# Performance work log

Measured on AMD Instinct MI355X. Metric: run time of the kernel, lower is better.

## Reference

```python
import jax, jax.numpy as jnp
import numpy as np
from jax import lax

# Static config (matches init_kwargs / electrode montage)
B, T, V = 16, 1536, 64
F1, D, H = 16, 2, 4
F2 = F1 * D              # 32
FO = F2 // H             # 8, GAT per-head out dim
K1, K3 = 32, 16          # conv kernel sizes (temporal)
P1, P2 = 8, 4            # avg pool sizes
KNN = 4
EPS = 1e-5
NEG_SLOPE = 0.2          # PyG GATConv leaky_relu slope


def _build_edges():
    # deterministic electrode geometry -> kNN graph, plus PyG self-loops
    rng = np.random.RandomState(0)
    pos = rng.randn(V, 3)
    dmat = np.linalg.norm(pos[:, None] - pos[None, :], axis=-1)
    order = np.argsort(dmat, axis=1)
    nbrs = order[:, 1:KNN + 1]                      # exclude self
    src = np.repeat(np.arange(V), KNN)
    dst = nbrs.reshape(-1)
    # add self loops (GATConv default add_self_loops=True)
    src = np.concatenate([src, np.arange(V)])
    dst = np.concatenate([dst, np.arange(V)])
    return jnp.asarray(np.stack([src, dst]), dtype=jnp.int32)  # (2, E)


def _bn(x, g, b, m, v, axis):
    shp = [1] * x.ndim
    shp[axis] = -1
    rs = lambda a: a.reshape(shp)
    return rs(g) * (x - rs(m)) * lax.rsqrt(rs(v) + EPS) + rs(b)


def _conv_same_t(x, w, k):
    # Conv2d(..., (1,k), padding='same'): torch pads (k-1)//2 left, rest right
    lp = (k - 1) // 2
    return lax.conv_general_dilated(x, w, (1, 1), [(0, 0), (lp, k - 1 - lp)],
                                    dimension_numbers=('NCHW', 'OIHW', 'NCHW'))


def _gat(x, W, a_src, a_dst, bias, src, dst):
    # Batched PyG GATConv (eval mode, dropout off), concat heads.
    # x: (Ng, V, F1); W: (F1, H*FO); a_src/a_dst: (H, FO); bias: (H*FO,)
    Ng = x.shape[0]
    h = jnp.einsum('nvf,fho->nvho', x, W.reshape(F1, H, FO))   # (Ng,V,H,FO)
    es = jnp.einsum('nvho,ho->nvh', h, a_src)[:, src]          # (Ng,E,H)
    ed = jnp.einsum('nvho,ho->nvh', h, a_dst)[:, dst]
    e = jax.nn.leaky_relu(es + ed, NEG_SLOPE)
    # softmax over incoming edges of each target node (segment softmax)
    m = jnp.full((Ng, V, H), -1e30, e.dtype).at[:, dst].max(e)
    ex = jnp.exp(e - m[:, dst])
    den = jnp.zeros((Ng, V, H), e.dtype).at[:, dst].add(ex)
    alpha = ex / den[:, dst]                                   # (Ng,E,H)
    out = jnp.zeros((Ng, V, H, FO), e.dtype).at[:, dst].add(alpha[..., None] * h[:, src])
    return out.reshape(Ng, V, H * FO) + bias


def setup_inputs() -> dict:
    key = jax.random.key(0)
    ks = jax.random.split(key, 16)
    bn = lambda k, c: (1.0 + 0.1 * jax.random.normal(jax.random.fold_in(k, 0), (c,)),
                       0.1 * jax.random.normal(jax.random.fold_in(k, 1), (c,)),
                       0.1 * jax.random.normal(jax.random.fold_in(k, 2), (c,)),
                       0.5 + jax.random.uniform(jax.random.fold_in(k, 3), (c,)))
    bn1 = bn(ks[1], F1); bn2 = bn(ks[2], F2); bn3 = bn(ks[3], F2)
    inp = {
        'x': jax.random.normal(ks[0], (B, 1, V, T), jnp.float32),
        'conv1_w': 0.1 * jax.random.normal(ks[4], (F1, 1, 1, K1), jnp.float32),
        'bn1_g': bn1[0], 'bn1_b': bn1[1], 'bn1_m': bn1[2], 'bn1_v': bn1[3],
        'gat_w': (1.0 / np.sqrt(F1)) * jax.random.normal(ks[5], (F1, H * FO), jnp.float32),
        'gat_asrc': 0.3 * jax.random.normal(ks[6], (H, FO), jnp.float32),
        'gat_adst': 0.3 * jax.random.normal(ks[7], (H, FO), jnp.float32),
        'gat_bias': 0.05 * jax.random.normal(ks[8], (H * FO,), jnp.float32),
        'bn2_g': bn2[0], 'bn2_b': bn2[1], 'bn2_m': bn2[2], 'bn2_v': bn2[3],
        'conv3_w': 0.1 * jax.random.normal(ks[9], (F2, F2, 1, K3), jnp.float32),
        'bn3_g': bn3[0], 'bn3_b': bn3[1], 'bn3_m': bn3[2], 'bn3_v': bn3[3],
        'edge_index': _build_edges(),
    }
    return inp


def reference(x, conv1_w, bn1_g, bn1_b, bn1_m, bn1_v,
              gat_w, gat_asrc, gat_adst, gat_bias,
              bn2_g, bn2_b, bn2_m, bn2_v,
              conv3_w, bn3_g, bn3_b, bn3_m, bn3_v, edge_index):
    src, dst = edge_index[0], edge_index[1]
    # block1: temporal conv + BN
    h = _conv_same_t(x, conv1_w, K1)                 # (B,F1,V,T)
    h = _bn(h, bn1_g, bn1_b, bn1_m, bn1_v, 1)
    # spatial GNN over B*T independent electrode graphs
    xg = h.transpose(0, 3, 2, 1).reshape(B * T, V, F1)
    g = _gat(xg, gat_w, gat_asrc, gat_adst, gat_bias, src, dst)   # (BT,V,F2)
    g = g.mean(axis=1).reshape(B, T, F2).transpose(0, 2, 1)       # (B,F2,T)
    g = _bn(g, bn2_g, bn2_b, bn2_m, bn2_v, 1)[:, :, None, :]      # (B,F2,1,T)
    # tail: elu -> pool -> conv -> bn -> elu -> pool (dropout = eval no-op)
    h = jax.nn.elu(g)
    h = h.reshape(B, F2, 1, T // P1, P1).mean(-1)
    h = _conv_same_t(h, conv3_w, K3)
    h = _bn(h, bn3_g, bn3_b, bn3_m, bn3_v, 1)
    h = jax.nn.elu(h)
    h = h.reshape(B, F2, 1, T // P1 // P2, P2).mean(-1)           # (B,F2,1,48)
    return h
```

## Files before the change

### kernel.cpp

```cpp
#include <hip/hip_runtime.h>
#include <math.h>

#define TPB 256

constexpr int Bc = 16, Tc = 1536;
constexpr int T2c = 192;
constexpr float EPSc = 1e-5f;
constexpr float NSLOPE = 0.2f;
constexpr int MDI = 16;
constexpr int MDO = 8;
constexpr int NOUT = 5;
constexpr float L2E = 1.4426950408889634f;

typedef float vf2 __attribute__((ext_vector_type(2)));

constexpr int OW_WEFF = 0;
constexpr int OW_CHL  = 1024;
constexpr int OW_CES  = 1056;
constexpr int OW_WES  = 1064;
constexpr int OW_WED  = 1192;
constexpr int OW_A2C2 = 1320;
constexpr int OW_WFT  = 1384;
constexpr int OW_GRAPH= 2408;
constexpr int OW_P    = 2825;

constexpr int GB_INTS = 417;

constexpr int L_XT  = 0;
constexpr int L_WB  = 2720;
constexpr int L_Y   = 4896;
constexpr int L_GR  = 6208;
constexpr int L_TOT = 6625;

__global__ void prep_kernel(const float* __restrict__ c1w,
                            const float* __restrict__ g1, const float* __restrict__ b1,
                            const float* __restrict__ m1, const float* __restrict__ v1,
                            const float* __restrict__ W,
                            const float* __restrict__ asrc, const float* __restrict__ adst,
                            const float* __restrict__ bias,
                            const float* __restrict__ g2, const float* __restrict__ b2,
                            const float* __restrict__ m2, const float* __restrict__ v2,
                            const int* __restrict__ ei, int ne, float* __restrict__ ws)
{
    const int tid = threadIdx.x;
    __shared__ float sweff[1024];
    __shared__ float schl[32];
    __shared__ int isrcp_i[64 * MDI];
    __shared__ int outdst_i[64 * MDO];
    __shared__ int inslot[64], outslot[64];

    for (int idx = tid; idx < 1024; idx += TPB) {
        int k = idx >> 5, f2 = idx & 31;
        float s = 0.f;
        for (int f = 0; f < 16; f++) {
            float a1 = g1[f] * rsqrtf(v1[f] + EPSc);
            s += a1 * W[f * 32 + f2] * c1w[f * 32 + k];
        }
        ws[OW_WEFF + idx] = s;
        ws[OW_WFT + f2 * 32 + k] = s;
        sweff[idx] = s;
    }
    for (int f2 = tid; f2 < 32; f2 += TPB) {
        float s = 0.f;
        for (int f = 0; f < 16; f++) {
            float a1 = g1[f] * rsqrtf(v1[f] + EPSc);
            s = fmaf(b1[f] - a1 * m1[f], W[f * 32 + f2], s);
        }
        ws[OW_CHL + f2] = s;
        schl[f2] = s;
        float a2 = g2[f2] * rsqrtf(v2[f2] + EPSc);
        ws[OW_A2C2 + f2] = a2;
        ws[OW_A2C2 + 32 + f2] = b2[f2] + a2 * (bias[f2] - m2[f2]);
    }

    for (int i = tid; i < 64 * MDI; i += TPB) isrcp_i[i] = 0;
    for (int i = tid; i < 64 * MDO; i += TPB) outdst_i[i] = 0;
    if (tid < 64) { inslot[tid] = 0; outslot[tid] = 0; }
    __syncthreads();
    for (int e = tid; e < ne; e += TPB) {
        int s = ei[e], d = ei[ne + e];
        int pi = atomicAdd(&inslot[d], 1);
        if (pi < MDI) isrcp_i[d * MDI + pi] = s;
        int po = atomicAdd(&outslot[s], 1);
        if (po < MDO) outdst_i[s * MDO + po] = d;
    }
    __syncthreads();

    if (tid < 128) {
        int k = tid >> 2, h = tid & 3;
        float s1 = 0.f, s2 = 0.f;
        for (int o = 0; o < 8; o++) {
            float wv = sweff[k * 32 + h * 8 + o];
            s1 = fmaf(asrc[h * 8 + o], wv, s1);
            s2 = fmaf(adst[h * 8 + o], wv, s2);
        }
        ws[OW_WES + h * 32 + k] = s1;
        ws[OW_WED + h * 32 + k] = s2;
    }
    if (tid < 4) {
        float s1 = 0.f, s2 = 0.f;
        for (int o = 0; o < 8; o++) {
            float cv = schl[tid * 8 + o];
            s1 = fmaf(asrc[tid * 8 + o], cv, s1);
            s2 = fmaf(adst[tid * 8 + o], cv, s2);
        }
        ws[OW_CES + tid] = s1;
        ws[OW_CES + 4 + tid] = s2;
    }
    unsigned char* gb = (unsigned char*)(ws + OW_GRAPH);
    for (int i = tid; i < 64 * MDI; i += TPB) gb[i] = (unsigned char)isrcp_i[i];
    for (int i = tid; i < 64 * MDO; i += TPB) gb[1088 + i] = (unsigned char)outdst_i[i];
    if (tid < 64) {
        gb[1024 + tid] = (unsigned char)(inslot[tid] < MDI ? inslot[tid] : MDI);
        gb[1600 + tid] = (unsigned char)(outslot[tid] < MDO ? outslot[tid] : MDO);
    }
    __syncthreads();
    if (tid == 0) {
        int mi = 0, mo = 0;
        for (int d = 0; d < 64; d++) {
            int a = gb[1024 + d], o = gb[1600 + d];
            mi = a > mi ? a : mi;
            mo = o > mo ? o : mo;
        }
        gb[1664] = (unsigned char)mi;
        gb[1665] = (unsigned char)mo;
    }
}

__global__ __launch_bounds__(TPB, 4) void gat_kernel(
    const float* __restrict__ x,
    const float* __restrict__ wfTp,
    const float* __restrict__ chlp,
    const float* __restrict__ cesg,
    const float* __restrict__ wesg,
    const float* __restrict__ wedg,
    const float* __restrict__ a2c2,
    const int* __restrict__ graphi,
    float* __restrict__ pout)
{
    __shared__ __align__(16) float sm[L_TOT];
    unsigned char* gb = (unsigned char*)&sm[L_GR];

    const int tid  = threadIdx.x;
    const int b    = blockIdx.x / 192;
    const int tile = blockIdx.x % 192;
    const int t0   = tile * 8;

    const int h = tid >> 6, v = tid & 63;

    for (int idx = tid; idx < GB_INTS; idx += TPB) ((int*)&sm[L_GR])[idx] = graphi[idx];
    for (int idx = tid; idx < 2560; idx += TPB) {
        const int vv = idx / 40, j = idx % 40;
        float val = 1.0f;
        if (j < 39) {
            const int t = t0 - 15 + j;
            val = (t >= 0 && t < Tc) ? x[(b * 64 + vv) * Tc + t] : 0.f;
        }
        sm[L_XT + j * 68 + vv] = val;
    }
    __syncthreads();

    const int hs = __builtin_amdgcn_readfirstlane(h);
    const float* wesh = wesg + hs * 32;
    const float* wedh = wedg + hs * 32;

    float aes[8], aed[8];
    {
        const float cesh = cesg[hs], cedh = cesg[4 + hs];
        #pragma unroll
        for (int t = 0; t < 8; t++) { aes[t] = cesh; aed[t] = cedh; }
        float xr[8];
        #pragma unroll
        for (int q = 0; q < 7; q++) xr[q] = sm[L_XT + q * 68 + v];
        #pragma unroll
        for (int k = 0; k < 32; k++) {
            xr[(k + 7) & 7] = sm[L_XT + (k + 7) * 68 + v];
            const float wek = wesh[k];
            const float wdk = wedh[k];
            #pragma unroll
            for (int t = 0; t < 8; t++) {
                const float xv = xr[(k + t) & 7];
                aes[t] = fmaf(xv, wek, aes[t]);
                aed[t] = fmaf(xv, wdk, aed[t]);
            }
        }
    }

    {
        vf2 aes2[4], aed2[4];
        #pragma unroll
        for (int tp = 0; tp < 4; tp++) {
            aes2[tp] = (vf2){aes[2 * tp] * L2E, aes[2 * tp + 1] * L2E};
            aed2[tp] = (vf2){aed[2 * tp] * L2E, aed[2 * tp + 1] * L2E};
        }
        const vf2 ns2 = (vf2){NSLOPE, NSLOPE};

        const int indeg = gb[1024 + v];
        const int mdin  = gb[1664];
        vf2 den2[4] = {(vf2){0.f,0.f},(vf2){0.f,0.f},(vf2){0.f,0.f},(vf2){0.f,0.f}};
        for (int e = 0; e < mdin; e++) {
            const int s = gb[v * MDI + e];
            const float valid = (e < indeg) ? 1.f : 0.f;
            #pragma unroll
            for (int tp = 0; tp < 4; tp++) {
                unsigned long long pv =
                    __shfl(__builtin_bit_cast(unsigned long long, aes2[tp]), s);
                vf2 sv = __builtin_bit_cast(vf2, pv);
                vf2 ev = sv + aed2[tp];
                vf2 em = ev * ns2;
                float e0 = fmaxf(ev.x, em.x);
                float e1 = fmaxf(ev.y, em.y);
                den2[tp].x += valid * __builtin_amdgcn_exp2f(e0);
                den2[tp].y += valid * __builtin_amdgcn_exp2f(e1);
            }
        }
        vf2 rden2[4];
        #pragma unroll
        for (int tp = 0; tp < 4; tp++) {
            float dx = den2[tp].x, dy = den2[tp].y;
            float rx = __builtin_amdgcn_rcpf(dx); rx = rx * (2.f - dx * rx);
            float ry = __builtin_amdgcn_rcpf(dy); ry = ry * (2.f - dy * ry);
            rden2[tp] = (vf2){rx, ry};
        }

        vf2 wb2[4] = {(vf2){0.f,0.f},(vf2){0.f,0.f},(vf2){0.f,0.f},(vf2){0.f,0.f}};
        #pragma unroll
        for (int j = 0; j < NOUT; j++) {
            const int d = gb[1088 + v * MDO + j];
            #pragma unroll
            for (int tp = 0; tp < 4; tp++) {
                vf2 dv = __builtin_bit_cast(vf2,
                    (unsigned long long)__shfl(__builtin_bit_cast(unsigned long long, aed2[tp]), d));
                vf2 ev = aes2[tp] + dv;
                vf2 em = ev * ns2;
                float Ex = __builtin_amdgcn_exp2f(fmaxf(ev.x, em.x));
                float Ey = __builtin_amdgcn_exp2f(fmaxf(ev.y, em.y));
                vf2 rv = __builtin_bit_cast(vf2,
                    (unsigned long long)__shfl(__builtin_bit_cast(unsigned long long, rden2[tp]), d));
                wb2[tp].x = fmaf(Ex, rv.x, wb2[tp].x);
                wb2[tp].y = fmaf(Ey, rv.y, wb2[tp].y);
            }
        }
        #pragma unroll
        for (int tp = 0; tp < 4; tp++) {
            sm[L_WB + h * 544 + (2 * tp) * 68 + v]     = wb2[tp].x;
            sm[L_WB + h * 544 + (2 * tp + 1) * 68 + v] = wb2[tp].y;
        }
    }
    __asm__ volatile("s_waitcnt lgkmcnt(0)" ::: "memory");

    {
        const int vh = v >> 5, tp = (v >> 3) & 3, cg = v & 7;
        vf2 yp[2][5];
        #pragma unroll
        for (int i = 0; i < 2; i++)
            #pragma unroll
            for (int q = 0; q < 5; q++)
                yp[i][q] = (vf2){0.f, 0.f};
        const float* xbase = &sm[L_XT + cg * 5 * 68 + vh * 32];
        const float* wb0   = &sm[L_WB + h * 544 + (2 * tp) * 68 + vh * 32];
        #pragma unroll
        for (int v4 = 0; v4 < 8; v4++) {
            const float4 wa  = *(const float4*)(wb0 + v4 * 4);
            const float4 wbv = *(const float4*)(wb0 + 68 + v4 * 4);
            const vf2 wa01 = (vf2){wa.x, wa.y},  wa23 = (vf2){wa.z, wa.w};
            const vf2 wv01 = (vf2){wbv.x, wbv.y}, wv23 = (vf2){wbv.z, wbv.w};
            #pragma unroll
            for (int q = 0; q < 5; q++) {
                const float4 x4 = *(const float4*)(xbase + q * 68 + v4 * 4);
                const vf2 x01 = (vf2){x4.x, x4.y}, x23 = (vf2){x4.z, x4.w};
                yp[0][q] += wa01 * x01;
                yp[0][q] += wa23 * x23;
                yp[1][q] += wv01 * x01;
                yp[1][q] += wv23 * x23;
            }
        }
        float ya[2][5];
        #pragma unroll
        for (int i = 0; i < 2; i++)
            #pragma unroll
            for (int q = 0; q < 5; q++) {
                ya[i][q] = yp[i][q].x + yp[i][q].y;
                ya[i][q] += __shfl_xor(ya[i][q], 32);
            }
        if (vh == 0) {
            float* yr = &sm[L_Y + h * 328 + (2 * tp) * 41 + cg * 5];
            #pragma unroll
            for (int i = 0; i < 2; i++)
                #pragma unroll
                for (int q = 0; q < 5; q++)
                    yr[i * 41 + q] = ya[i][q];
        }
    }
    __asm__ volatile("s_waitcnt lgkmcnt(0)" ::: "memory");

    {
        const int t = v >> 3, o = v & 7;
        const int f2d = h * 8 + o;
        const float4* wf4 = (const float4*)(wfTp + f2d * 32);

        const float* yr = &sm[L_Y + h * 328 + t * 41];
        float acc = chlp[f2d] * yr[39];
        #pragma unroll
        for (int k4 = 0; k4 < 8; k4++) {
            const float4 w = wf4[k4];
            acc = fmaf(w.x, yr[t + 4 * k4 + 0],
                  fmaf(w.y, yr[t + 4 * k4 + 1],
                  fmaf(w.z, yr[t + 4 * k4 + 2],
                  fmaf(w.w, yr[t + 4 * k4 + 3], acc))));
        }

        const float a2 = a2c2[f2d], c2 = a2c2[32 + f2d];
        float y = fmaf(a2, acc * (1.f / 64.f), c2);
        y = y > 0.f ? y : __expf(y) - 1.f;
        y += __shfl_xor(y, 8);
        y += __shfl_xor(y, 16);
        y += __shfl_xor(y, 32);
        if (v < 8)
            pout[(b * T2c + tile) * 32 + h * 8 + v] = y * 0.125f;
    }
}

__global__ __launch_bounds__(TPB) void conv3_kernel(const float* __restrict__ pp,
                                                    const float* __restrict__ w3,
                                                    const float* __restrict__ g3,
                                                    const float* __restrict__ b3,
                                                    const float* __restrict__ m3,
                                                    const float* __restrict__ v3,
                                                    float* __restrict__ outp)
{
    __shared__ float pl[63 * 32];
    __shared__ float q[48 * 32];
    const int tid = threadIdx.x;
    const int b = blockIdx.x >> 2, cc = blockIdx.x & 3;

    for (int idx = tid; idx < 63 * 32; idx += TPB) {
        int r = idx >> 5, f2 = idx & 31;
        int tog = cc * 48 - 7 + r;
        pl[idx] = (tog >= 0 && tog < T2c) ? pp[(b * T2c + tog) * 32 + f2] : 0.f;
    }
    __syncthreads();

    const int f2o = tid & 31, grp = tid >> 5;
    const int tb = grp * 6;
    float acc[6] = { 0.f, 0.f, 0.f, 0.f, 0.f, 0.f };
    for (int f2i = 0; f2i < 32; f2i++) {
        float seg[21];
        #pragma unroll
        for (int r = 0; r < 21; r++) seg[r] = pl[(tb + r) * 32 + f2i];
        const float4* wrow = (const float4*)(w3 + (f2o * 32 + f2i) * 16);
        #pragma unroll
        for (int k4 = 0; k4 < 4; k4++) {
            const float4 w4 = wrow[k4];
            #pragma unroll
            for (int j = 0; j < 6; j++) {
                acc[j] = fmaf(seg[j + k4 * 4 + 0], w4.x,
                         fmaf(seg[j + k4 * 4 + 1], w4.y,
                         fmaf(seg[j + k4 * 4 + 2], w4.z,
                         fmaf(seg[j + k4 * 4 + 3], w4.w, acc[j]))));
            }
        }
    }
    const float a3 = g3[f2o] * rsqrtf(v3[f2o] + EPSc);
    const float c3 = b3[f2o] - a3 * m3[f2o];
    #pragma unroll
    for (int j = 0; j < 6; j++) {
        float y = fmaf(a3, acc[j], c3);
        y = y > 0.f ? y : __expf(y) - 1.f;
        q[(tb + j) * 32 + f2o] = y;
    }
    __syncthreads();
    for (int idx = tid; idx < 12 * 32; idx += TPB) {
        int t4 = idx >> 5, f2 = idx & 31;
        int r0 = t4 * 4;
        float s = q[r0 * 32 + f2] + q[(r0 + 1) * 32 + f2] +
                  q[(r0 + 2) * 32 + f2] + q[(r0 + 3) * 32 + f2];
        outp[(b * 32 + f2) * 48 + cc * 12 + t4] = s * 0.25f;
    }
}

extern "C" void kernel_launch(void* const* d_in, const int* in_sizes, int n_in,
                              void* d_out, int out_size, void* d_ws, size_t ws_size,
                              hipStream_t stream)
{
    const float* x    = (const float*)d_in[0];
    const float* c1w  = (const float*)d_in[1];
    const float* g1   = (const float*)d_in[2];
    const float* b1   = (const float*)d_in[3];
    const float* m1   = (const float*)d_in[4];
    const float* v1   = (const float*)d_in[5];
    const float* W    = (const float*)d_in[6];
    const float* asrc = (const float*)d_in[7];
    const float* adst = (const float*)d_in[8];
    const float* bias = (const float*)d_in[9];
    const float* g2   = (const float*)d_in[10];
    const float* b2   = (const float*)d_in[11];
    const float* m2   = (const float*)d_in[12];
    const float* v2   = (const float*)d_in[13];
    const float* w3   = (const float*)d_in[14];
    const float* g3   = (const float*)d_in[15];
    const float* b3   = (const float*)d_in[16];
    const float* m3   = (const float*)d_in[17];
    const float* v3   = (const float*)d_in[18];
    const int*   ei   = (const int*)d_in[19];
    const int    ne   = in_sizes[19] / 2;

    float* ws = (float*)d_ws;

    prep_kernel<<<1, TPB, 0, stream>>>(c1w, g1, b1, m1, v1, W, asrc, adst,
                                       bias, g2, b2, m2, v2, ei, ne, ws);

    gat_kernel<<<Bc * T2c, TPB, 0, stream>>>(x,
                                             ws + OW_WFT, ws + OW_CHL,
                                             ws + OW_CES,
                                             ws + OW_WES, ws + OW_WED,
                                             ws + OW_A2C2,
                                             (const int*)(ws + OW_GRAPH),
                                             ws + OW_P);

    conv3_kernel<<<Bc * 4, TPB, 0, stream>>>(ws + OW_P, w3, g3, b3, m3, v3,
                                             (float*)d_out);
}
```

Measured before the change: 161.9 us.

## Swizzle x tile LDS layout, split self-loops out of GAT softmax, repartition aggregation

The x tile in shared memory now uses an XOR-style swizzled column layout so the float4 reads in the aggregation stage avoid bank conflicts. Self-loop edges are dropped from the adjacency lists and handled directly, so the neighbor loop no longer shuffles for them. The edge loop is fully unrolled with packed byte indices loaded as an int4, and out-edges are fixed at 4. The aggregation is repartitioned so each thread computes 4 weight rows over 16 vertices with an extra shuffle reduction. This depends on every node having exactly 4 out-edges plus a self-loop, which holds for the kNN graph but would break for other graphs.

```diff
diff --git a/kernel.cpp b/kernel.cpp
--- a/kernel.cpp
+++ b/kernel.cpp
@@ -9,7 +9,6 @@
 constexpr float NSLOPE = 0.2f;
 constexpr int MDI = 16;
 constexpr int MDO = 8;
-constexpr int NOUT = 5;
 constexpr float L2E = 1.4426950408889634f;
 
 typedef float vf2 __attribute__((ext_vector_type(2)));
@@ -32,6 +31,29 @@
 constexpr int L_GR  = 6208;
 constexpr int L_TOT = 6625;
 
+__device__ __forceinline__ int xt_idx(int row, int g, int lo)
+{
+    return L_XT + row * 68 + (((g + row) & 15) << 2) + lo;
+}
+
+__device__ __forceinline__ vf2 shfl64v(vf2 xv, int src)
+{
+    return __builtin_bit_cast(vf2,
+        (unsigned long long)__shfl(__builtin_bit_cast(unsigned long long, xv), src));
+}
+
+__device__ __forceinline__ vf2 lexp2v(vf2 ev)
+{
+    vf2 em = ev * (vf2){NSLOPE, NSLOPE};
+    return (vf2){__builtin_amdgcn_exp2f(fmaxf(ev.x, em.x)),
+                 __builtin_amdgcn_exp2f(fmaxf(ev.y, em.y))};
+}
+
+__device__ __forceinline__ float bfly32_sum(float s)
+{
+    return s + __shfl_xor(s, 32);
+}
+
 __global__ void prep_kernel(const float* __restrict__ c1w,
                             const float* __restrict__ g1, const float* __restrict__ b1,
                             const float* __restrict__ m1, const float* __restrict__ v1,
@@ -79,8 +101,9 @@
     __syncthreads();
     for (int e = tid; e < ne; e += TPB) {
         int s = ei[e], d = ei[ne + e];
+        if (s == d) continue;
         int pi = atomicAdd(&inslot[d], 1);
-        if (pi < MDI) isrcp_i[d * MDI + pi] = s;
+        if (pi < 15) isrcp_i[d * MDI + pi] = s;
         int po = atomicAdd(&outslot[s], 1);
         if (po < MDO) outdst_i[s * MDO + po] = d;
     }
@@ -110,20 +133,23 @@
     unsigned char* gb = (unsigned char*)(ws + OW_GRAPH);
     for (int i = tid; i < 64 * MDI; i += TPB) gb[i] = (unsigned char)isrcp_i[i];
     for (int i = tid; i < 64 * MDO; i += TPB) gb[1088 + i] = (unsigned char)outdst_i[i];
+    __syncthreads();
     if (tid < 64) {
-        gb[1024 + tid] = (unsigned char)(inslot[tid] < MDI ? inslot[tid] : MDI);
-        gb[1600 + tid] = (unsigned char)(outslot[tid] < MDO ? outslot[tid] : MDO);
+        int id = inslot[tid] < 15 ? inslot[tid] : 15;
+        int od = outslot[tid] < MDO ? outslot[tid] : MDO;
+        gb[tid * MDI + 15] = (unsigned char)id;
+        gb[1024 + tid] = (unsigned char)id;
+        gb[1600 + tid] = (unsigned char)od;
     }
     __syncthreads();
     if (tid == 0) {
-        int mi = 0, mo = 0;
+        int mi = 0;
         for (int d = 0; d < 64; d++) {
-            int a = gb[1024 + d], o = gb[1600 + d];
+            int a = gb[1024 + d];
             mi = a > mi ? a : mi;
-            mo = o > mo ? o : mo;
         }
         gb[1664] = (unsigned char)mi;
-        gb[1665] = (unsigned char)mo;
+        gb[1665] = 0;
     }
 }
 
@@ -156,7 +182,7 @@
             const int t = t0 - 15 + j;
             val = (t >= 0 && t < Tc) ? x[(b * 64 + vv) * Tc + t] : 0.f;
         }
-        sm[L_XT + j * 68 + vv] = val;
+        sm[xt_idx(j, vv >> 2, vv & 3)] = val;
     }
     __syncthreads();
 
@@ -166,15 +192,16 @@
 
     float aes[8], aed[8];
     {
+        const int g = v >> 2, lo = v & 3;
         const float cesh = cesg[hs], cedh = cesg[4 + hs];
         #pragma unroll
         for (int t = 0; t < 8; t++) { aes[t] = cesh; aed[t] = cedh; }
         float xr[8];
         #pragma unroll
-        for (int q = 0; q < 7; q++) xr[q] = sm[L_XT + q * 68 + v];
+        for (int q = 0; q < 7; q++) xr[q] = sm[xt_idx(q, g, lo)];
         #pragma unroll
         for (int k = 0; k < 32; k++) {
-            xr[(k + 7) & 7] = sm[L_XT + (k + 7) * 68 + v];
+            xr[(k + 7) & 7] = sm[xt_idx(k + 7, g, lo)];
             const float wek = wesh[k];
             const float wdk = wedh[k];
             #pragma unroll
@@ -193,52 +220,54 @@
             aes2[tp] = (vf2){aes[2 * tp] * L2E, aes[2 * tp + 1] * L2E};
             aed2[tp] = (vf2){aed[2 * tp] * L2E, aed[2 * tp + 1] * L2E};
         }
-        const vf2 ns2 = (vf2){NSLOPE, NSLOPE};
-
-        const int indeg = gb[1024 + v];
-        const int mdin  = gb[1664];
-        vf2 den2[4] = {(vf2){0.f,0.f},(vf2){0.f,0.f},(vf2){0.f,0.f},(vf2){0.f,0.f}};
-        for (int e = 0; e < mdin; e++) {
-            const int s = gb[v * MDI + e];
-            const float valid = (e < indeg) ? 1.f : 0.f;
-            #pragma unroll
-            for (int tp = 0; tp < 4; tp++) {
-                unsigned long long pv =
-                    __shfl(__builtin_bit_cast(unsigned long long, aes2[tp]), s);
-                vf2 sv = __builtin_bit_cast(vf2, pv);
-                vf2 ev = sv + aed2[tp];
-                vf2 em = ev * ns2;
-                float e0 = fmaxf(ev.x, em.x);
-                float e1 = fmaxf(ev.y, em.y);
-                den2[tp].x += valid * __builtin_amdgcn_exp2f(e0);
-                den2[tp].y += valid * __builtin_amdgcn_exp2f(e1);
-            }
-        }
-        vf2 rden2[4];
+
+        const int4 il = *(const int4*)(gb + v * MDI);
+        const unsigned ow = *(const unsigned*)(gb + 1088 + v * MDO);
+        const int indeg = ((unsigned)il.w) >> 24;
+        int mdin = gb[1664];
+        mdin = __builtin_amdgcn_readfirstlane(mdin);
+        const unsigned iw[4] = {(unsigned)il.x, (unsigned)il.y,
+                                (unsigned)il.z, (unsigned)il.w};
+
+        vf2 Es2[4], den2[4];
+        #pragma unroll
+        for (int tp = 0; tp < 4; tp++) {
+            Es2[tp] = lexp2v(aes2[tp] + aed2[tp]);
+            den2[tp] = Es2[tp];
+        }
+        #pragma unroll
+        for (int e = 0; e < 15; e++) {
+            if (e < mdin) {
+                const int s = (iw[e >> 2] >> ((e & 3) * 8)) & 0xFF;
+                const float valid = (e < indeg) ? 1.f : 0.f;
+                #pragma unroll
+                for (int tp = 0; tp < 4; tp++) {
+                    vf2 ev = shfl64v(aes2[tp], s) + aed2[tp];
+                    vf2 E = lexp2v(ev);
+                    den2[tp].x += valid * E.x;
+                    den2[tp].y += valid * E.y;
+                }
+            }
+        }
+        vf2 rden2[4], wb2[4];
         #pragma unroll
         for (int tp = 0; tp < 4; tp++) {
             float dx = den2[tp].x, dy = den2[tp].y;
             float rx = __builtin_amdgcn_rcpf(dx); rx = rx * (2.f - dx * rx);
             float ry = __builtin_amdgcn_rcpf(dy); ry = ry * (2.f - dy * ry);
             rden2[tp] = (vf2){rx, ry};
-        }
-
-        vf2 wb2[4] = {(vf2){0.f,0.f},(vf2){0.f,0.f},(vf2){0.f,0.f},(vf2){0.f,0.f}};
-        #pragma unroll
-        for (int j = 0; j < NOUT; j++) {
-            const int d = gb[1088 + v * MDO + j];
+            wb2[tp] = Es2[tp] * rden2[tp];
+        }
+        #pragma unroll
+        for (int j = 0; j < 4; j++) {
+            const int d = (ow >> (j * 8)) & 0xFF;
             #pragma unroll
             for (int tp = 0; tp < 4; tp++) {
-                vf2 dv = __builtin_bit_cast(vf2,
-                    (unsigned long long)__shfl(__builtin_bit_cast(unsigned long long, aed2[tp]), d));
-                vf2 ev = aes2[tp] + dv;
-                vf2 em = ev * ns2;
-                float Ex = __builtin_amdgcn_exp2f(fmaxf(ev.x, em.x));
-                float Ey = __builtin_amdgcn_exp2f(fmaxf(ev.y, em.y));
-                vf2 rv = __builtin_bit_cast(vf2,
-                    (unsigned long long)__shfl(__builtin_bit_cast(unsigned long long, rden2[tp]), d));
-                wb2[tp].x = fmaf(Ex, rv.x, wb2[tp].x);
-                wb2[tp].y = fmaf(Ey, rv.y, wb2[tp].y);
+                vf2 ev = aes2[tp] + shfl64v(aed2[tp], d);
+                vf2 E = lexp2v(ev);
+                vf2 rv = shfl64v(rden2[tp], d);
+                wb2[tp].x = fmaf(E.x, rv.x, wb2[tp].x);
+                wb2[tp].y = fmaf(E.y, rv.y, wb2[tp].y);
             }
         }
         #pragma unroll
@@ -250,46 +279,54 @@
     __asm__ volatile("s_waitcnt lgkmcnt(0)" ::: "memory");
 
     {
-        const int vh = v >> 5, tp = (v >> 3) & 3, cg = v & 7;
-        vf2 yp[2][5];
-        #pragma unroll
-        for (int i = 0; i < 2; i++)
-            #pragma unroll
-            for (int q = 0; q < 5; q++)
-                yp[i][q] = (vf2){0.f, 0.f};
-        const float* xbase = &sm[L_XT + cg * 5 * 68 + vh * 32];
-        const float* wb0   = &sm[L_WB + h * 544 + (2 * tp) * 68 + vh * 32];
-        #pragma unroll
-        for (int v4 = 0; v4 < 8; v4++) {
-            const float4 wa  = *(const float4*)(wb0 + v4 * 4);
-            const float4 wbv = *(const float4*)(wb0 + 68 + v4 * 4);
-            const vf2 wa01 = (vf2){wa.x, wa.y},  wa23 = (vf2){wa.z, wa.w};
-            const vf2 wv01 = (vf2){wbv.x, wbv.y}, wv23 = (vf2){wbv.z, wbv.w};
+        const int cg = v & 7;
+        const int th = (v >> 3) & 1;
+        const int kq = v >> 4;
+
+        vf2 yp[4][5];
+        #pragma unroll
+        for (int i = 0; i < 4; i++)
+            #pragma unroll
+            for (int q = 0; q < 5; q++) yp[i][q] = (vf2){0.f, 0.f};
+
+        const float* wbbase = &sm[L_WB + h * 544 + (th * 4) * 68];
+        #pragma unroll
+        for (int v4 = 0; v4 < 4; v4++) {
+            const int vcol = kq * 16 + v4 * 4;
+            float4 wrow[4];
+            #pragma unroll
+            for (int i = 0; i < 4; i++)
+                wrow[i] = *(const float4*)(wbbase + i * 68 + vcol);
             #pragma unroll
             for (int q = 0; q < 5; q++) {
-                const float4 x4 = *(const float4*)(xbase + q * 68 + v4 * 4);
+                const int row = cg * 5 + q;
+                const int mg = ((kq * 4 + v4 + row) & 15) << 2;
+                const float4 x4 = *(const float4*)(&sm[L_XT + row * 68 + mg]);
                 const vf2 x01 = (vf2){x4.x, x4.y}, x23 = (vf2){x4.z, x4.w};
-                yp[0][q] += wa01 * x01;
-                yp[0][q] += wa23 * x23;
-                yp[1][q] += wv01 * x01;
-                yp[1][q] += wv23 * x23;
-            }
-        }
-        float ya[2][5];
-        #pragma unroll
-        for (int i = 0; i < 2; i++)
+                #pragma unroll
+                for (int i = 0; i < 4; i++) {
+                    const vf2 w01 = (vf2){wrow[i].x, wrow[i].y};
+                    const vf2 w23 = (vf2){wrow[i].z, wrow[i].w};
+                    yp[i][q] += w01 * x01;
+                    yp[i][q] += w23 * x23;
+                }
+            }
+        }
+        float ya[4][5];
+        #pragma unroll
+        for (int i = 0; i < 4; i++)
             #pragma unroll
             for (int q = 0; q < 5; q++) {
-                ya[i][q] = yp[i][q].x + yp[i][q].y;
-                ya[i][q] += __shfl_xor(ya[i][q], 32);
-            }
-        if (vh == 0) {
-            float* yr = &sm[L_Y + h * 328 + (2 * tp) * 41 + cg * 5];
-            #pragma unroll
-            for (int i = 0; i < 2; i++)
-                #pragma unroll
-                for (int q = 0; q < 5; q++)
-                    yr[i * 41 + q] = ya[i][q];
+                float s = yp[i][q].x + yp[i][q].y;
+                s += __shfl_xor(s, 16);
+                ya[i][q] = bfly32_sum(s);
+            }
+        float* yw = &sm[L_Y + h * 328 + (th * 4 + kq) * 41 + cg * 5];
+        #pragma unroll
+        for (int q = 0; q < 5; q++) {
+            float a01 = (kq & 1) ? ya[1][q] : ya[0][q];
+            float a23 = (kq & 1) ? ya[3][q] : ya[2][q];
+            yw[q] = (kq & 2) ? a23 : a01;
         }
     }
     __asm__ volatile("s_waitcnt lgkmcnt(0)" ::: "memory");
@@ -315,7 +352,7 @@
         y = y > 0.f ? y : __expf(y) - 1.f;
         y += __shfl_xor(y, 8);
         y += __shfl_xor(y, 16);
-        y += __shfl_xor(y, 32);
+        y = bfly32_sum(y);
         if (v < 8)
             pout[(b * T2c + tile) * 32 + h * 8 + v] = y * 0.125f;
     }
```

Measured after the change: 168.0 us. 3.8% more time.
